# Performance work log

Hardware: AMD Instinct MI355X
Metric: run time of the kernel (lower is better)

The kernel has to match this reference:

```python
import jax, jax.numpy as jnp
import numpy as np

N_NODES = 50000
N_EDGES = 300000
N_GRAPHS = 256
F_IN = 78
H1 = 10
F_H1 = 78
F_OUT = 128
NEG_SLOPE = 0.2  # PyG GATConv default leaky_relu slope


def gat_conv(x, src, dst, W, a_src, a_dst, bias, heads, out_dim):
    """PyG GATConv (eval mode): linear -> per-edge attention -> segment softmax over
    destination nodes -> scatter-add aggregation -> concat heads + bias.
    src/dst already include self-loops."""
    N = x.shape[0]
    h = (x @ W).reshape(N, heads, out_dim)              # [N,H,F]
    al_s = (h * a_src[None]).sum(-1)                     # [N,H]
    al_d = (h * a_dst[None]).sum(-1)                     # [N,H]
    e = jax.nn.leaky_relu(al_s[src] + al_d[dst], NEG_SLOPE)  # [E,H]
    m = jax.ops.segment_max(e, dst, num_segments=N)      # stable softmax per dst node
    w = jnp.exp(e - m[dst])
    denom = jax.ops.segment_sum(w, dst, num_segments=N)
    alpha = w / denom[dst]                               # [E,H]
    out = jax.ops.segment_sum(h[src] * alpha[:, :, None], dst, num_segments=N)
    return out.reshape(N, heads * out_dim) + bias


def setup_inputs() -> dict:
    key = jax.random.key(0)
    ks = jax.random.split(key, 16)
    x = jax.random.normal(ks[0], (N_NODES, F_IN), dtype=jnp.float32)
    edge_index = jax.random.randint(ks[1], (2, N_EDGES), 0, N_NODES, dtype=jnp.int32)
    batch = jnp.sort(jax.random.randint(ks[2], (N_NODES,), 0, N_GRAPHS, dtype=jnp.int32))
    s = 0.1
    W1 = jax.random.normal(ks[3], (F_IN, H1 * F_H1), dtype=jnp.float32) * s
    a_src1 = jax.random.normal(ks[4], (H1, F_H1), dtype=jnp.float32) * s
    a_dst1 = jax.random.normal(ks[5], (H1, F_H1), dtype=jnp.float32) * s
    b1 = jnp.zeros((H1 * F_H1,), dtype=jnp.float32)
    W2 = jax.random.normal(ks[6], (H1 * F_H1, F_OUT), dtype=jnp.float32) * s
    a_src2 = jax.random.normal(ks[7], (1, F_OUT), dtype=jnp.float32) * s
    a_dst2 = jax.random.normal(ks[8], (1, F_OUT), dtype=jnp.float32) * s
    b2 = jnp.zeros((F_OUT,), dtype=jnp.float32)
    fc_w = jax.random.normal(ks[9], (F_OUT, F_OUT), dtype=jnp.float32) * s
    fc_b = jnp.zeros((F_OUT,), dtype=jnp.float32)
    return dict(x=x, edge_index=edge_index, batch=batch, W1=W1, a_src1=a_src1,
                a_dst1=a_dst1, b1=b1, W2=W2, a_src2=a_src2, a_dst2=a_dst2, b2=b2,
                fc_w=fc_w, fc_b=fc_b)


def reference(x, edge_index, batch, W1, a_src1, a_dst1, b1, W2, a_src2, a_dst2, b2, fc_w, fc_b):
    N = x.shape[0]
    loop = jnp.arange(N, dtype=edge_index.dtype)
    src = jnp.concatenate([edge_index[0], loop])  # add self-loops (PyG default)
    dst = jnp.concatenate([edge_index[1], loop])
    # dropout layers are identity in eval mode
    h = jax.nn.elu(gat_conv(x, src, dst, W1, a_src1, a_dst1, b1, H1, F_H1))
    h = gat_conv(h, src, dst, W2, a_src2, a_dst2, b2, 1, F_OUT)
    h = jax.nn.relu(h)
    g = jax.ops.segment_max(h, batch, num_segments=N_GRAPHS)  # global max pool [B,F]
    out = jax.nn.relu(g @ fc_w + fc_b)
    return out
```

## Files before the change

### kernel.cpp

```cpp
#include <hip/hip_runtime.h>
#include <hip/hip_bf16.h>

#define N_NODES 50000
#define N_EDGES 300000
#define E_TOT   350000
#define N_GRAPHS 256
#define F_IN 78
#define H1 10
#define D1 780
#define F_OUT 128
#define KP 800
#define K1P 96
#define NEG_SLOPE 0.2f
#define NB 196

typedef float v4f __attribute__((ext_vector_type(4)));
typedef short v8s __attribute__((ext_vector_type(8)));

__device__ __forceinline__ int src_of(int e, const int* __restrict__ ei) {
  return (e < N_EDGES) ? ei[e] : (e - N_EDGES);
}
__device__ __forceinline__ int dst_of(int e, const int* __restrict__ ei) {
  return (e < N_EDGES) ? ei[N_EDGES + e] : (e - N_EDGES);
}


__global__ void k_deg(const int* __restrict__ ei, int* __restrict__ deg) {
  int e = blockIdx.x * 256 + threadIdx.x;
  if (e >= E_TOT) return;
  atomicAdd(&deg[dst_of(e, ei)], 1);
}

__global__ void k_scan1(const int* __restrict__ deg, int* __restrict__ part) {
  __shared__ int s[256];
  int t = threadIdx.x;
  int i = blockIdx.x * 256 + t;
  s[t] = (i < N_NODES) ? deg[i] : 0;
  __syncthreads();
  for (int d = 128; d > 0; d >>= 1) {
    if (t < d) s[t] += s[t + d];
    __syncthreads();
  }
  if (t == 0) part[blockIdx.x] = s[0];
}

__global__ void k_scan2(const int* __restrict__ part, int* __restrict__ ppref) {
  if (threadIdx.x == 0) {
    int run = 0;
    for (int i = 0; i < NB; ++i) { ppref[i] = run; run += part[i]; }
  }
}

__global__ void k_scan3(const int* __restrict__ deg, const int* __restrict__ ppref,
                        int* __restrict__ offs, int* __restrict__ cursor) {
  __shared__ int s[256];
  int t = threadIdx.x;
  int i = blockIdx.x * 256 + t;
  int v = (i < N_NODES) ? deg[i] : 0;
  s[t] = v;
  __syncthreads();
  for (int d = 1; d < 256; d <<= 1) {
    int u = (t >= d) ? s[t - d] : 0;
    __syncthreads();
    s[t] += u;
    __syncthreads();
  }
  int excl = s[t] - v;
  if (i < N_NODES) {
    int off = ppref[blockIdx.x] + excl;
    offs[i] = off;
    cursor[i] = off;
  }
}

__global__ void k_scatter(const int* __restrict__ ei, int* __restrict__ cursor,
                          int* __restrict__ src_s, int* __restrict__ dst_s) {
  int e = blockIdx.x * 256 + threadIdx.x;
  if (e >= E_TOT) return;
  int s = src_of(e, ei);
  int d = dst_of(e, ei);
  int pos = atomicAdd(&cursor[d], 1);
  src_s[pos] = s;
  dst_s[pos] = d;
}


__global__ void k_prep(const float* __restrict__ W1, const float* __restrict__ as1,
                       const float* __restrict__ ad1, float* __restrict__ was,
                       float* __restrict__ wad) {
  int i = blockIdx.x * 256 + threadIdx.x;
  if (i >= F_IN * H1) return;
  int k = i / H1, h = i - k * H1;
  const float* wrow = W1 + (size_t)k * D1 + h * 78;
  const float* ar = as1 + h * 78;
  const float* br = ad1 + h * 78;
  float s = 0.f, d = 0.f;
  for (int f = 0; f < 78; ++f) {
    float w = wrow[f];
    s = fmaf(w, ar[f], s);
    d = fmaf(w, br[f], d);
  }
  was[i] = s;
  wad[i] = d;
}


__global__ __launch_bounds__(320) void k_logits1(const float* __restrict__ x,
                                                 const float* __restrict__ was,
                                                 const float* __restrict__ wad,
                                                 float* __restrict__ als,
                                                 float* __restrict__ ald) {
  __shared__ float xs[32][81];
  __shared__ float wl[D1], wl2[D1];
  int tid = threadIdx.x;
  int n0 = blockIdx.x * 32;
  for (int i = tid; i < 32 * F_IN; i += 320) {
    int r = i / F_IN, k = i - r * F_IN;
    int n = n0 + r;
    xs[r][k] = (n < N_NODES) ? x[(size_t)n * F_IN + k] : 0.f;
  }
  for (int i = tid; i < D1; i += 320) { wl[i] = was[i]; wl2[i] = wad[i]; }
  __syncthreads();
  int r = tid / 10, h = tid - r * 10;
  int n = n0 + r;
  float s = 0.f, d = 0.f;
  for (int k = 0; k < F_IN; ++k) {
    float xv = xs[r][k];
    s = fmaf(xv, wl[k * 10 + h], s);
    d = fmaf(xv, wl2[k * 10 + h], d);
  }
  if (n < N_NODES) { als[n * 10 + h] = s; ald[n * 10 + h] = d; }
}


__global__ void k_w1e(const float* __restrict__ als1, const float* __restrict__ ald1,
                      const int* __restrict__ src_s, const int* __restrict__ dst_s,
                      float* __restrict__ w1) {
  int i = blockIdx.x * 256 + threadIdx.x;
  if (i >= E_TOT * H1) return;
  int pos = i / H1, h = i - pos * H1;
  float v = als1[src_s[pos] * H1 + h] + ald1[dst_s[pos] * H1 + h];
  v = (v > 0.f) ? v : NEG_SLOPE * v;
  w1[i] = __expf(v);
}


__global__ void k_w1t(const float* __restrict__ W1, __hip_bfloat16* __restrict__ T) {
  int i = blockIdx.x * 256 + threadIdx.x;
  if (i >= 800 * K1P) return;
  int r = i / K1P, k = i - r * K1P;
  float v = (r < D1 && k < F_IN) ? W1[(size_t)k * D1 + r] : 0.f;
  T[i] = __float2bfloat16(v);
}


__global__ __launch_bounds__(512, 4) void k_agg1f(const float* __restrict__ x,
                                                  const float* __restrict__ w1,
                                                  const int* __restrict__ src_s,
                                                  const int* __restrict__ offs,
                                                  const int* __restrict__ deg,
                                                  const __hip_bfloat16* __restrict__ W1T,
                                                  const float* __restrict__ b1,
                                                  __hip_bfloat16* __restrict__ out1) {
  __shared__ __hip_bfloat16 xb[H1][16][104];
  int tid = threadIdx.x, wid = tid >> 6, lane = tid & 63;
  int n0 = blockIdx.x * 16;

  {
    unsigned int* p = (unsigned int*)xb;
    for (int i = tid; i < H1 * 16 * 52; i += 512) p[i] = 0u;
  }
  __syncthreads();

  #pragma unroll
  for (int rep = 0; rep < 2; ++rep) {
    int g = wid * 2 + rep;
    int n = n0 + g;
    int o = __builtin_amdgcn_readfirstlane(offs[n]);
    int d = __builtin_amdgcn_readfirstlane(deg[n]);
    float acc[H1], acc2[H1];
    #pragma unroll
    for (int h = 0; h < H1; ++h) { acc[h] = 0.f; acc2[h] = 0.f; }

    int j = 0;
    for (; j + 2 <= d; j += 2) {
      int e0 = o + j, e1 = o + j + 1;
      int s0 = src_s[e0], s1 = src_s[e1];
      const float* x0 = x + (size_t)s0 * F_IN;
      const float* x1 = x + (size_t)s1 * F_IN;
      float xa0 = x0[lane];
      float xa1 = x1[lane];
      float xb0 = (lane < 14) ? x0[64 + lane] : ((lane == 14) ? 1.0f : 0.f);
      float xb1 = (lane < 14) ? x1[64 + lane] : ((lane == 14) ? 1.0f : 0.f);
      const float* wp0 = w1 + (size_t)e0 * H1;
      const float* wp1 = w1 + (size_t)e1 * H1;
      #pragma unroll
      for (int h = 0; h < H1; ++h) {
        float wa = wp0[h], wb = wp1[h];
        acc[h] = fmaf(wa, xa0, acc[h]);
        acc[h] = fmaf(wb, xa1, acc[h]);
        acc2[h] = fmaf(wa, xb0, acc2[h]);
        acc2[h] = fmaf(wb, xb1, acc2[h]);
      }
    }
    if (j < d) {
      int e0 = o + j;
      int s0 = src_s[e0];
      const float* x0 = x + (size_t)s0 * F_IN;
      float xa0 = x0[lane];
      float xb0 = (lane < 14) ? x0[64 + lane] : ((lane == 14) ? 1.0f : 0.f);
      const float* wp0 = w1 + (size_t)e0 * H1;
      #pragma unroll
      for (int h = 0; h < H1; ++h) {
        float wa = wp0[h];
        acc[h] = fmaf(wa, xa0, acc[h]);
        acc2[h] = fmaf(wa, xb0, acc2[h]);
      }
    }
    #pragma unroll
    for (int h = 0; h < H1; ++h) {
      float inv = 1.f / __shfl(acc2[h], 14);
      xb[h][g][lane] = __float2bfloat16(acc[h] * inv);
      if (lane < 14) xb[h][g][64 + lane] = __float2bfloat16(acc2[h] * inv);
    }
  }
  __syncthreads();

  const unsigned short* Bp = (const unsigned short*)W1T;
  int col16 = lane & 15, kq = (lane >> 4) * 8;
  for (int u = wid; u < 50; u += 8) {
    int h = u / 5, nt = u - (u / 5) * 5;
    v4f acc = (v4f){0.f, 0.f, 0.f, 0.f};
    #pragma unroll
    for (int kt = 0; kt < 3; ++kt) {
      v8s a = *reinterpret_cast<const v8s*>(&xb[h][col16][kt * 32 + kq]);
      v8s b = *reinterpret_cast<const v8s*>(
          &Bp[(size_t)(h * 78 + nt * 16 + col16) * K1P + kt * 32 + kq]);
      acc = __builtin_amdgcn_mfma_f32_16x16x32_bf16(a, b, acc, 0, 0, 0);
    }
    int cl = nt * 16 + col16;
    if (cl < 78) {
      int c = h * 78 + cl;
      float bv = b1[c];
      #pragma unroll
      for (int r = 0; r < 4; ++r) {
        int node = (lane >> 4) * 4 + r;
        float v = acc[r] + bv;
        v = (v > 0.f) ? v : expm1f(v);
        out1[(size_t)(n0 + node) * D1 + c] = __float2bfloat16(v);
      }
    }
  }
}


__global__ void k_w2t(const float* __restrict__ W2, __hip_bfloat16* __restrict__ Bt) {
  int i = blockIdx.x * 256 + threadIdx.x;
  if (i >= F_OUT * KP) return;
  int c = i / KP, k = i - c * KP;
  float v = (k < D1) ? W2[(size_t)k * F_OUT + c] : 0.f;
  Bt[i] = __float2bfloat16(v);
}


__global__ __launch_bounds__(256) void k_gemm2m(const __hip_bfloat16* __restrict__ A,
                                                const __hip_bfloat16* __restrict__ Bt,
                                                float* __restrict__ C) {
  int tid = threadIdx.x;
  int wid = tid >> 6, lane = tid & 63;
  int wr = wid >> 1, wc = wid & 1;
  int m0 = blockIdx.x * 64;
  int row16 = lane & 15, kchunk = (lane >> 4) * 8;
  v4f acc[2][4];
  #pragma unroll
  for (int ri = 0; ri < 2; ++ri)
    #pragma unroll
    for (int nf = 0; nf < 4; ++nf) acc[ri][nf] = (v4f){0.f, 0.f, 0.f, 0.f};

  const unsigned short* Ap = (const unsigned short*)A;
  const unsigned short* Bp = (const unsigned short*)Bt;

  for (int k0 = 0; k0 < KP; k0 += 32) {
    int ka = k0 + kchunk;
    v8s a[2], b[4];
    #pragma unroll
    for (int ri = 0; ri < 2; ++ri) {
      const unsigned short* p = Ap + (size_t)(m0 + wr * 32 + ri * 16 + row16) * D1 + ka;
      union { uint2 q[2]; v8s v; } u;
      u.q[0] = *reinterpret_cast<const uint2*>(p);
      u.q[1] = *reinterpret_cast<const uint2*>(p + 4);
      a[ri] = u.v;
    }
    #pragma unroll
    for (int nf = 0; nf < 4; ++nf) {
      const unsigned short* p = Bp + (size_t)(wc * 64 + nf * 16 + row16) * KP + ka;
      b[nf] = *reinterpret_cast<const v8s*>(p);
    }
    #pragma unroll
    for (int ri = 0; ri < 2; ++ri)
      #pragma unroll
      for (int nf = 0; nf < 4; ++nf)
        acc[ri][nf] = __builtin_amdgcn_mfma_f32_16x16x32_bf16(a[ri], b[nf], acc[ri][nf], 0, 0, 0);
  }
  #pragma unroll
  for (int ri = 0; ri < 2; ++ri) {
    int rbase = m0 + wr * 32 + ri * 16 + (lane >> 4) * 4;
    #pragma unroll
    for (int r = 0; r < 4; ++r) {
      int gm = rbase + r;
      if (gm < N_NODES) {
        #pragma unroll
        for (int nf = 0; nf < 4; ++nf)
          C[(size_t)gm * F_OUT + wc * 64 + nf * 16 + (lane & 15)] = acc[ri][nf][r];
      }
    }
  }
}


__global__ __launch_bounds__(64) void k_al2(const float* __restrict__ h2,
                                            const float* __restrict__ asrc,
                                            const float* __restrict__ adst,
                                            float* __restrict__ als,
                                            float* __restrict__ ald) {
  int n = blockIdx.x, lane = threadIdx.x;
  const float* hp = h2 + (size_t)n * F_OUT;
  float h0 = hp[lane], h64 = hp[64 + lane];
  float s = h0 * asrc[lane] + h64 * asrc[64 + lane];
  float d = h0 * adst[lane] + h64 * adst[64 + lane];
  #pragma unroll
  for (int off = 32; off > 0; off >>= 1) {
    s += __shfl_down(s, off);
    d += __shfl_down(d, off);
  }
  if (lane == 0) { als[n] = s; ald[n] = d; }
}


__global__ void k_w2e(const float* __restrict__ als2, const float* __restrict__ ald2,
                      const int* __restrict__ src_s, const int* __restrict__ dst_s,
                      float* __restrict__ w2) {
  int pos = blockIdx.x * 256 + threadIdx.x;
  if (pos >= E_TOT) return;
  float v = als2[src_s[pos]] + ald2[dst_s[pos]];
  v = (v > 0.f) ? v : NEG_SLOPE * v;
  w2[pos] = __expf(v);
}


__global__ __launch_bounds__(512) void k_agg2f(const float* __restrict__ h2,
                                               const float* __restrict__ w2,
                                               const int* __restrict__ src_s,
                                               const int* __restrict__ offs,
                                               const int* __restrict__ deg,
                                               const float* __restrict__ b2,
                                               const int* __restrict__ batch,
                                               unsigned int* __restrict__ g) {
  int tid = threadIdx.x;
  int n = blockIdx.x * 4 + (tid >> 7);
  int f = tid & 127;
  int o = __builtin_amdgcn_readfirstlane(offs[n]);
  int d = __builtin_amdgcn_readfirstlane(deg[n]);
  float acc = 0.f, ssum = 0.f;
  int j = 0;
  for (; j + 4 <= d; j += 4) {
    float wq[4], hq[4];
    #pragma unroll
    for (int q = 0; q < 4; ++q) {
      int e = o + j + q;
      wq[q] = w2[e];
      hq[q] = h2[(size_t)src_s[e] * F_OUT + f];
    }
    #pragma unroll
    for (int q = 0; q < 4; ++q) {
      ssum += wq[q];
      acc = fmaf(wq[q], hq[q], acc);
    }
  }
  for (; j < d; ++j) {
    int e = o + j;
    float w = w2[e];
    ssum += w;
    acc = fmaf(w, h2[(size_t)src_s[e] * F_OUT + f], acc);
  }
  float v = fmaxf(acc / ssum + b2[f], 0.f);
  int gc = __builtin_amdgcn_readfirstlane(batch[n]);
  atomicMax(&g[gc * F_OUT + f], __float_as_uint(v));
}


__global__ __launch_bounds__(128) void k_fc(const float* __restrict__ g,
                                            const float* __restrict__ fc_w,
                                            const float* __restrict__ fc_b,
                                            float* __restrict__ out) {
  int b = blockIdx.x, c = threadIdx.x;
  const float* gr = g + (size_t)b * F_OUT;
  float acc = 0.f;
  for (int k = 0; k < F_OUT; ++k) acc = fmaf(gr[k], fc_w[k * F_OUT + c], acc);
  float v = acc + fc_b[c];
  out[(size_t)b * F_OUT + c] = fmaxf(v, 0.f);
}


extern "C" void kernel_launch(void* const* d_in, const int* in_sizes, int n_in,
                              void* d_out, int out_size, void* d_ws, size_t ws_size,
                              hipStream_t stream) {
  const float* x      = (const float*)d_in[0];
  const int*   ei     = (const int*)  d_in[1];
  const int*   batch  = (const int*)  d_in[2];
  const float* W1     = (const float*)d_in[3];
  const float* a_src1 = (const float*)d_in[4];
  const float* a_dst1 = (const float*)d_in[5];
  const float* b1     = (const float*)d_in[6];
  const float* W2     = (const float*)d_in[7];
  const float* a_src2 = (const float*)d_in[8];
  const float* a_dst2 = (const float*)d_in[9];
  const float* b2     = (const float*)d_in[10];
  const float* fc_w   = (const float*)d_in[11];
  const float* fc_b   = (const float*)d_in[12];
  float* out = (float*)d_out;

  float* ws = (float*)d_ws;
  __hip_bfloat16* out1 = (__hip_bfloat16*)ws;
  float* h2   = ws + 19501000;
  float* als1 = ws + 25901000;
  float* ald1 = ws + 26401000;
  float* als2 = ws + 26901000;
  float* ald2 = ws + 26951000;
  float* g    = ws + 27001000;
  float* was  = ws + 27034000;
  float* wad  = ws + 27035000;
  __hip_bfloat16* W2T = (__hip_bfloat16*)(ws + 27036000);
  __hip_bfloat16* W1T = (__hip_bfloat16*)(ws + 27088000);
  float* w1   = ws + 27127000;
  float* w2   = ws + 30627000;
  int* ib     = (int*)(ws + 30977000);
  int* deg    = ib;
  int* offs   = ib + 50000;
  int* cursor = ib + 100000;
  int* src_s  = ib + 150000;
  int* dst_s  = ib + 500000;
  int* part   = ib + 850000;
  int* ppref  = ib + 850224;

  hipMemsetAsync(deg, 0, N_NODES * sizeof(int), stream);
  k_deg<<<(E_TOT + 255) / 256, 256, 0, stream>>>(ei, deg);
  k_scan1<<<NB, 256, 0, stream>>>(deg, part);
  k_scan2<<<1, 64, 0, stream>>>(part, ppref);
  k_scan3<<<NB, 256, 0, stream>>>(deg, ppref, offs, cursor);
  k_scatter<<<(E_TOT + 255) / 256, 256, 0, stream>>>(ei, cursor, src_s, dst_s);

  k_prep<<<4, 256, 0, stream>>>(W1, a_src1, a_dst1, was, wad);
  k_w1t<<<(800 * K1P + 255) / 256, 256, 0, stream>>>(W1, W1T);
  k_w2t<<<(F_OUT * KP + 255) / 256, 256, 0, stream>>>(W2, W2T);
  hipMemsetAsync((char*)out1 + (size_t)N_NODES * D1 * 2, 0, 2048, stream);
  hipMemsetAsync(g, 0, N_GRAPHS * F_OUT * sizeof(float), stream);

  k_logits1<<<(N_NODES + 31) / 32, 320, 0, stream>>>(x, was, wad, als1, ald1);
  k_w1e<<<(E_TOT * H1 + 255) / 256, 256, 0, stream>>>(als1, ald1, src_s, dst_s, w1);
  k_agg1f<<<N_NODES / 16, 512, 0, stream>>>(x, w1, src_s, offs, deg, W1T, b1, out1);

  k_gemm2m<<<(N_NODES + 63) / 64, 256, 0, stream>>>(out1, W2T, h2);
  k_al2<<<N_NODES, 64, 0, stream>>>(h2, a_src2, a_dst2, als2, ald2);
  k_w2e<<<(E_TOT + 255) / 256, 256, 0, stream>>>(als2, ald2, src_s, dst_s, w2);
  k_agg2f<<<(N_NODES + 3) / 4, 512, 0, stream>>>(h2, w2, src_s, offs, deg, b2, batch, (unsigned int*)g);

  k_fc<<<N_GRAPHS, F_OUT, 0, stream>>>(g, fc_w, fc_b, out);
}
```

Measured before the change: 297.3 us.

## Fuse layer-1 aggregation, layer-2 GEMM and attention logits into one kernel

Merges the layer-1 aggregation/projection kernel with the layer-2 GEMM and the per-node attention-logit kernel. The ELU output tile for 16 nodes now stays in LDS as bf16 and feeds the W2 MFMA directly, and h2 is also kept in LDS to compute als2/ald2. This avoids writing and re-reading the 78MB out1 intermediate and drops two launches. The cost is that each block redoes a small GEMM that streams all of W2T, and LDS use per block goes up. It also unrolls the edge gather loop by four instead of two.

```diff
diff --git a/kernel.cpp b/kernel.cpp
--- a/kernel.cpp
+++ b/kernel.cpp
@@ -154,20 +154,40 @@
 }
 
 
-__global__ __launch_bounds__(512, 4) void k_agg1f(const float* __restrict__ x,
-                                                  const float* __restrict__ w1,
-                                                  const int* __restrict__ src_s,
-                                                  const int* __restrict__ offs,
-                                                  const int* __restrict__ deg,
-                                                  const __hip_bfloat16* __restrict__ W1T,
-                                                  const float* __restrict__ b1,
-                                                  __hip_bfloat16* __restrict__ out1) {
-  __shared__ __hip_bfloat16 xb[H1][16][104];
+__global__ void k_w2t(const float* __restrict__ W2, __hip_bfloat16* __restrict__ Bt) {
+  int i = blockIdx.x * 256 + threadIdx.x;
+  if (i >= F_OUT * KP) return;
+  int c = i / KP, k = i - c * KP;
+  float v = (k < D1) ? W2[(size_t)k * F_OUT + c] : 0.f;
+  Bt[i] = __float2bfloat16(v);
+}
+
+
+__global__ __launch_bounds__(512, 4) void k_l12(const float* __restrict__ x,
+                                                const float* __restrict__ w1,
+                                                const int* __restrict__ src_s,
+                                                const int* __restrict__ offs,
+                                                const int* __restrict__ deg,
+                                                const __hip_bfloat16* __restrict__ W1T,
+                                                const float* __restrict__ b1,
+                                                const __hip_bfloat16* __restrict__ W2T,
+                                                const float* __restrict__ a_src2,
+                                                const float* __restrict__ a_dst2,
+                                                float* __restrict__ h2,
+                                                float* __restrict__ als2,
+                                                float* __restrict__ ald2) {
+  __shared__ __align__(16) unsigned char lds[33792];
+  __hip_bfloat16* xbb = (__hip_bfloat16*)lds;
+  __hip_bfloat16* out1t = (__hip_bfloat16*)lds;
+  float* h2t = (float*)(lds + 25600);
+#define XB(h, g, k) xbb[((h) * 16 + (g)) * 104 + (k)]
+
   int tid = threadIdx.x, wid = tid >> 6, lane = tid & 63;
   int n0 = blockIdx.x * 16;
+  int col16 = lane & 15, kq = (lane >> 4) * 8;
 
   {
-    unsigned int* p = (unsigned int*)xb;
+    unsigned int* p = (unsigned int*)lds;
     for (int i = tid; i < H1 * 16 * 52; i += 512) p[i] = 0u;
   }
   __syncthreads();
@@ -182,37 +202,44 @@
     #pragma unroll
     for (int h = 0; h < H1; ++h) { acc[h] = 0.f; acc2[h] = 0.f; }
 
+    float onesel = (lane == 14) ? 1.0f : 0.f;
     int j = 0;
-    for (; j + 2 <= d; j += 2) {
-      int e0 = o + j, e1 = o + j + 1;
-      int s0 = src_s[e0], s1 = src_s[e1];
+    for (; j + 4 <= d; j += 4) {
+      int e0 = o + j;
+      int s0 = src_s[e0], s1 = src_s[e0 + 1], s2 = src_s[e0 + 2], s3 = src_s[e0 + 3];
       const float* x0 = x + (size_t)s0 * F_IN;
       const float* x1 = x + (size_t)s1 * F_IN;
-      float xa0 = x0[lane];
-      float xa1 = x1[lane];
-      float xb0 = (lane < 14) ? x0[64 + lane] : ((lane == 14) ? 1.0f : 0.f);
-      float xb1 = (lane < 14) ? x1[64 + lane] : ((lane == 14) ? 1.0f : 0.f);
-      const float* wp0 = w1 + (size_t)e0 * H1;
-      const float* wp1 = w1 + (size_t)e1 * H1;
+      const float* x2 = x + (size_t)s2 * F_IN;
+      const float* x3 = x + (size_t)s3 * F_IN;
+      float xa0 = x0[lane], xa1 = x1[lane], xa2 = x2[lane], xa3 = x3[lane];
+      float xb0 = (lane < 14) ? x0[64 + lane] : onesel;
+      float xb1 = (lane < 14) ? x1[64 + lane] : onesel;
+      float xb2 = (lane < 14) ? x2[64 + lane] : onesel;
+      float xb3 = (lane < 14) ? x3[64 + lane] : onesel;
+      const float* wp = w1 + (size_t)e0 * H1;
       #pragma unroll
       for (int h = 0; h < H1; ++h) {
-        float wa = wp0[h], wb = wp1[h];
+        float wa = wp[h], wb = wp[10 + h], wc = wp[20 + h], wd = wp[30 + h];
         acc[h] = fmaf(wa, xa0, acc[h]);
         acc[h] = fmaf(wb, xa1, acc[h]);
+        acc[h] = fmaf(wc, xa2, acc[h]);
+        acc[h] = fmaf(wd, xa3, acc[h]);
         acc2[h] = fmaf(wa, xb0, acc2[h]);
         acc2[h] = fmaf(wb, xb1, acc2[h]);
+        acc2[h] = fmaf(wc, xb2, acc2[h]);
+        acc2[h] = fmaf(wd, xb3, acc2[h]);
       }
     }
-    if (j < d) {
+    for (; j < d; ++j) {
       int e0 = o + j;
       int s0 = src_s[e0];
       const float* x0 = x + (size_t)s0 * F_IN;
       float xa0 = x0[lane];
-      float xb0 = (lane < 14) ? x0[64 + lane] : ((lane == 14) ? 1.0f : 0.f);
-      const float* wp0 = w1 + (size_t)e0 * H1;
+      float xb0 = (lane < 14) ? x0[64 + lane] : onesel;
+      const float* wp = w1 + (size_t)e0 * H1;
       #pragma unroll
       for (int h = 0; h < H1; ++h) {
-        float wa = wp0[h];
+        float wa = wp[h];
         acc[h] = fmaf(wa, xa0, acc[h]);
         acc2[h] = fmaf(wa, xb0, acc2[h]);
       }
@@ -220,24 +247,37 @@
     #pragma unroll
     for (int h = 0; h < H1; ++h) {
       float inv = 1.f / __shfl(acc2[h], 14);
-      xb[h][g][lane] = __float2bfloat16(acc[h] * inv);
-      if (lane < 14) xb[h][g][64 + lane] = __float2bfloat16(acc2[h] * inv);
-    }
-  }
-  __syncthreads();
-
-  const unsigned short* Bp = (const unsigned short*)W1T;
-  int col16 = lane & 15, kq = (lane >> 4) * 8;
+      XB(h, g, lane) = __float2bfloat16(acc[h] * inv);
+      if (lane < 14) XB(h, g, 64 + lane) = __float2bfloat16(acc2[h] * inv);
+    }
+  }
+  __syncthreads();
+
+  const unsigned short* Bp1 = (const unsigned short*)W1T;
+  v4f res[7];
+  int nu = 0;
   for (int u = wid; u < 50; u += 8) {
     int h = u / 5, nt = u - (u / 5) * 5;
     v4f acc = (v4f){0.f, 0.f, 0.f, 0.f};
     #pragma unroll
     for (int kt = 0; kt < 3; ++kt) {
-      v8s a = *reinterpret_cast<const v8s*>(&xb[h][col16][kt * 32 + kq]);
+      v8s a = *reinterpret_cast<const v8s*>(&XB(h, col16, kt * 32 + kq));
       v8s b = *reinterpret_cast<const v8s*>(
-          &Bp[(size_t)(h * 78 + nt * 16 + col16) * K1P + kt * 32 + kq]);
+          &Bp1[(size_t)(h * 78 + nt * 16 + col16) * K1P + kt * 32 + kq]);
       acc = __builtin_amdgcn_mfma_f32_16x16x32_bf16(a, b, acc, 0, 0, 0);
     }
+    res[nu++] = acc;
+  }
+  __syncthreads();
+
+  if (tid < 160) {
+    int node = tid / 10, cc = (tid - node * 10) * 2;
+    *(unsigned int*)&out1t[node * 800 + 780 + cc] = 0u;
+  }
+  nu = 0;
+  for (int u = wid; u < 50; u += 8) {
+    int h = u / 5, nt = u - (u / 5) * 5;
+    v4f acc = res[nu++];
     int cl = nt * 16 + col16;
     if (cl < 78) {
       int c = h * 78 + cl;
@@ -247,93 +287,46 @@
         int node = (lane >> 4) * 4 + r;
         float v = acc[r] + bv;
         v = (v > 0.f) ? v : expm1f(v);
-        out1[(size_t)(n0 + node) * D1 + c] = __float2bfloat16(v);
+        out1t[node * 800 + c] = __float2bfloat16(v);
       }
     }
   }
-}
-
-
-__global__ void k_w2t(const float* __restrict__ W2, __hip_bfloat16* __restrict__ Bt) {
-  int i = blockIdx.x * 256 + threadIdx.x;
-  if (i >= F_OUT * KP) return;
-  int c = i / KP, k = i - c * KP;
-  float v = (k < D1) ? W2[(size_t)k * F_OUT + c] : 0.f;
-  Bt[i] = __float2bfloat16(v);
-}
-
-
-__global__ __launch_bounds__(256) void k_gemm2m(const __hip_bfloat16* __restrict__ A,
-                                                const __hip_bfloat16* __restrict__ Bt,
-                                                float* __restrict__ C) {
-  int tid = threadIdx.x;
-  int wid = tid >> 6, lane = tid & 63;
-  int wr = wid >> 1, wc = wid & 1;
-  int m0 = blockIdx.x * 64;
-  int row16 = lane & 15, kchunk = (lane >> 4) * 8;
-  v4f acc[2][4];
+  __syncthreads();
+
+  const unsigned short* Bp2 = (const unsigned short*)W2T;
+  v4f acc3 = (v4f){0.f, 0.f, 0.f, 0.f};
+  #pragma unroll 5
+  for (int kt = 0; kt < 25; ++kt) {
+    int k = kt * 32 + kq;
+    v8s a = *reinterpret_cast<const v8s*>(&out1t[col16 * 800 + k]);
+    v8s b = *reinterpret_cast<const v8s*>(&Bp2[(size_t)(wid * 16 + col16) * KP + k]);
+    acc3 = __builtin_amdgcn_mfma_f32_16x16x32_bf16(a, b, acc3, 0, 0, 0);
+  }
+  {
+    int col = wid * 16 + col16;
+    #pragma unroll
+    for (int r = 0; r < 4; ++r) {
+      int node = (lane >> 4) * 4 + r;
+      h2[(size_t)(n0 + node) * F_OUT + col] = acc3[r];
+      h2t[node * F_OUT + col] = acc3[r];
+    }
+  }
+  __syncthreads();
+
   #pragma unroll
-  for (int ri = 0; ri < 2; ++ri)
-    #pragma unroll
-    for (int nf = 0; nf < 4; ++nf) acc[ri][nf] = (v4f){0.f, 0.f, 0.f, 0.f};
-
-  const unsigned short* Ap = (const unsigned short*)A;
-  const unsigned short* Bp = (const unsigned short*)Bt;
-
-  for (int k0 = 0; k0 < KP; k0 += 32) {
-    int ka = k0 + kchunk;
-    v8s a[2], b[4];
-    #pragma unroll
-    for (int ri = 0; ri < 2; ++ri) {
-      const unsigned short* p = Ap + (size_t)(m0 + wr * 32 + ri * 16 + row16) * D1 + ka;
-      union { uint2 q[2]; v8s v; } u;
-      u.q[0] = *reinterpret_cast<const uint2*>(p);
-      u.q[1] = *reinterpret_cast<const uint2*>(p + 4);
-      a[ri] = u.v;
-    }
-    #pragma unroll
-    for (int nf = 0; nf < 4; ++nf) {
-      const unsigned short* p = Bp + (size_t)(wc * 64 + nf * 16 + row16) * KP + ka;
-      b[nf] = *reinterpret_cast<const v8s*>(p);
-    }
-    #pragma unroll
-    for (int ri = 0; ri < 2; ++ri)
-      #pragma unroll
-      for (int nf = 0; nf < 4; ++nf)
-        acc[ri][nf] = __builtin_amdgcn_mfma_f32_16x16x32_bf16(a[ri], b[nf], acc[ri][nf], 0, 0, 0);
-  }
-  #pragma unroll
-  for (int ri = 0; ri < 2; ++ri) {
-    int rbase = m0 + wr * 32 + ri * 16 + (lane >> 4) * 4;
-    #pragma unroll
-    for (int r = 0; r < 4; ++r) {
-      int gm = rbase + r;
-      if (gm < N_NODES) {
-        #pragma unroll
-        for (int nf = 0; nf < 4; ++nf)
-          C[(size_t)gm * F_OUT + wc * 64 + nf * 16 + (lane & 15)] = acc[ri][nf][r];
-      }
-    }
-  }
-}
-
-
-__global__ __launch_bounds__(64) void k_al2(const float* __restrict__ h2,
-                                            const float* __restrict__ asrc,
-                                            const float* __restrict__ adst,
-                                            float* __restrict__ als,
-                                            float* __restrict__ ald) {
-  int n = blockIdx.x, lane = threadIdx.x;
-  const float* hp = h2 + (size_t)n * F_OUT;
-  float h0 = hp[lane], h64 = hp[64 + lane];
-  float s = h0 * asrc[lane] + h64 * asrc[64 + lane];
-  float d = h0 * adst[lane] + h64 * adst[64 + lane];
-  #pragma unroll
-  for (int off = 32; off > 0; off >>= 1) {
-    s += __shfl_down(s, off);
-    d += __shfl_down(d, off);
-  }
-  if (lane == 0) { als[n] = s; ald[n] = d; }
+  for (int rep = 0; rep < 2; ++rep) {
+    int nn = wid * 2 + rep;
+    float v0 = h2t[nn * F_OUT + lane], v1 = h2t[nn * F_OUT + 64 + lane];
+    float s = v0 * a_src2[lane] + v1 * a_src2[64 + lane];
+    float dd = v0 * a_dst2[lane] + v1 * a_dst2[64 + lane];
+    #pragma unroll
+    for (int off = 32; off > 0; off >>= 1) {
+      s += __shfl_down(s, off);
+      dd += __shfl_down(dd, off);
+    }
+    if (lane == 0) { als2[n0 + nn] = s; ald2[n0 + nn] = dd; }
+  }
+#undef XB
 }
 
 
@@ -421,20 +414,19 @@
   float* out = (float*)d_out;
 
   float* ws = (float*)d_ws;
-  __hip_bfloat16* out1 = (__hip_bfloat16*)ws;
-  float* h2   = ws + 19501000;
-  float* als1 = ws + 25901000;
-  float* ald1 = ws + 26401000;
-  float* als2 = ws + 26901000;
-  float* ald2 = ws + 26951000;
-  float* g    = ws + 27001000;
-  float* was  = ws + 27034000;
-  float* wad  = ws + 27035000;
-  __hip_bfloat16* W2T = (__hip_bfloat16*)(ws + 27036000);
-  __hip_bfloat16* W1T = (__hip_bfloat16*)(ws + 27088000);
-  float* w1   = ws + 27127000;
-  float* w2   = ws + 30627000;
-  int* ib     = (int*)(ws + 30977000);
+  float* h2   = ws;
+  float* als1 = ws + 6400000;
+  float* ald1 = ws + 6900000;
+  float* als2 = ws + 7400000;
+  float* ald2 = ws + 7450000;
+  float* g    = ws + 7500000;
+  float* was  = ws + 7533000;
+  float* wad  = ws + 7534000;
+  __hip_bfloat16* W2T = (__hip_bfloat16*)(ws + 7535000);
+  __hip_bfloat16* W1T = (__hip_bfloat16*)(ws + 7587000);
+  float* w1   = ws + 7626000;
+  float* w2   = ws + 11126000;
+  int* ib     = (int*)(ws + 11476000);
   int* deg    = ib;
   int* offs   = ib + 50000;
   int* cursor = ib + 100000;
@@ -453,15 +445,14 @@
   k_prep<<<4, 256, 0, stream>>>(W1, a_src1, a_dst1, was, wad);
   k_w1t<<<(800 * K1P + 255) / 256, 256, 0, stream>>>(W1, W1T);
   k_w2t<<<(F_OUT * KP + 255) / 256, 256, 0, stream>>>(W2, W2T);
-  hipMemsetAsync((char*)out1 + (size_t)N_NODES * D1 * 2, 0, 2048, stream);
   hipMemsetAsync(g, 0, N_GRAPHS * F_OUT * sizeof(float), stream);
 
   k_logits1<<<(N_NODES + 31) / 32, 320, 0, stream>>>(x, was, wad, als1, ald1);
   k_w1e<<<(E_TOT * H1 + 255) / 256, 256, 0, stream>>>(als1, ald1, src_s, dst_s, w1);
-  k_agg1f<<<N_NODES / 16, 512, 0, stream>>>(x, w1, src_s, offs, deg, W1T, b1, out1);
-
-  k_gemm2m<<<(N_NODES + 63) / 64, 256, 0, stream>>>(out1, W2T, h2);
-  k_al2<<<N_NODES, 64, 0, stream>>>(h2, a_src2, a_dst2, als2, ald2);
+
+  k_l12<<<N_NODES / 16, 512, 0, stream>>>(x, w1, src_s, offs, deg, W1T, b1,
+                                          W2T, a_src2, a_dst2, h2, als2, ald2);
+
   k_w2e<<<(E_TOT + 255) / 256, 256, 0, stream>>>(als2, ald2, src_s, dst_s, w2);
   k_agg2f<<<(N_NODES + 3) / 4, 512, 0, stream>>>(h2, w2, src_s, offs, deg, b2, batch, (unsigned int*)g);
 
```

Result: faster. 269.7 us (-9.3%).
